# Performance work log

Hardware: AMD Instinct MI355X
Metric: run time of the kernel (lower is better)

The kernel has to match this reference:

```python
import jax, jax.numpy as jnp
import numpy as np

SCORE_THRESHOLD = 0.35
TARGET_CLASS_ID = 0.0
R = 4_194_304  # number of candidate detections (rois)


def setup_inputs() -> dict:
    key = jax.random.key(0)
    k1, k2, k3 = jax.random.split(key, 3)
    class_ids = jax.random.randint(k1, (R,), 0, 4).astype(jnp.float32)
    boxes = jax.random.uniform(k2, (R, 4), dtype=jnp.float32)
    scores = jax.random.uniform(k3, (R,), dtype=jnp.float32)
    detections = jnp.concatenate([class_ids[:, None], boxes, scores[:, None]], axis=1)[None]  # [1, R, 6]
    return {"detections": detections}


def _compact(data, mask):
    # Stable stream compaction with fixed output shape: valid rows moved to the
    # front (original order preserved), invalid tail zero-padded.
    # data: [R, D] float, mask: [R] bool  ->  ([R, D], n_valid)
    order = jnp.argsort(jnp.logical_not(mask), stable=True)  # valid (False-key) first
    sel = jnp.take(data, order, axis=0)
    n = jnp.sum(mask.astype(jnp.int32))
    keep = (jnp.arange(data.shape[0]) < n)[:, None]
    return jnp.where(keep, sel, jnp.zeros((), data.dtype)), n


def reference(detections):
    # detections: [1, R, 6] = [class_id, x1, y1, x2, y2, score]
    d = detections[0]
    class_ids = d[:, 0]
    scores = d[:, 5]
    valid = (class_ids == TARGET_CLASS_ID) & (scores >= SCORE_THRESHOLD)
    valid_full = scores >= SCORE_THRESHOLD

    sel, n = _compact(d, valid)
    # rois: zero class stub + xyxy (score dropped), [1, R, 5]; padded rows are all-zero
    rois = jnp.concatenate([jnp.zeros((d.shape[0], 1), d.dtype), sel[:, 1:5]], axis=1)[None]

    rois_full, n_full = _compact(d, valid_full)
    rois_full = rois_full[None]  # [1, R, 6]

    return rois, rois_full, n, n_full
```

## Files before the change

kernel.cpp:

```cpp
#include <hip/hip_runtime.h>

typedef unsigned int uint32;
typedef unsigned long long uint64;

#define BLOCK 256
#define IPT 16
#define CHUNK (BLOCK * IPT)
#define SCORE_THR 0.35f

__device__ inline void block_reduce2(uint32& a, uint32& b) {
    int tid = threadIdx.x;
    int wave = tid >> 6, lane = tid & 63;
    for (int off = 32; off > 0; off >>= 1) {
        a += __shfl_down(a, off, 64);
        b += __shfl_down(b, off, 64);
    }
    __shared__ uint32 ra[BLOCK / 64], rb[BLOCK / 64];
    if (lane == 0) { ra[wave] = a; rb[wave] = b; }
    __syncthreads();
    uint32 sa = 0, sb = 0;
    for (int w = 0; w < BLOCK / 64; ++w) { sa += ra[w]; sb += rb[w]; }
    a = sa; b = sb;
}

__global__ void count_kernel(const float* __restrict__ det,
                             uint32* __restrict__ c0, uint32* __restrict__ c1,
                             int R) {
    int tid = threadIdx.x;
    long long base = (long long)blockIdx.x * CHUNK;
    uint32 cnt0 = 0, cnt1 = 0;

    if (base + CHUNK <= R) {
        const float4* d4 = (const float4*)det + base * 6 / 4;
        for (int it = 0; it < IPT / 2; ++it) {
            const float4* p = d4 + (long long)it * (BLOCK * 3) + 3 * tid;
            float4 f0 = p[0], f1 = p[1], f2 = p[2];
            bool mA1 = (f1.y >= SCORE_THR);
            bool mA0 = mA1 && (f0.x == 0.0f);
            bool mB1 = (f2.w >= SCORE_THR);
            bool mB0 = mB1 && (f1.z == 0.0f);
            cnt1 += (mA1 ? 1u : 0u) + (mB1 ? 1u : 0u);
            cnt0 += (mA0 ? 1u : 0u) + (mB0 ? 1u : 0u);
        }
    } else {
        for (int i = 0; i < IPT; ++i) {
            long long row = base + (long long)i * BLOCK + tid;
            if (row < R) {
                float c = det[row * 6 + 0];
                float s = det[row * 6 + 5];
                bool m1 = (s >= SCORE_THR);
                bool m0 = m1 && (c == 0.0f);
                cnt1 += m1 ? 1u : 0u;
                cnt0 += m0 ? 1u : 0u;
            }
        }
    }

    block_reduce2(cnt0, cnt1);
    if (tid == 0) { c0[blockIdx.x] = cnt0; c1[blockIdx.x] = cnt1; }
}

__global__ void scatter_zero_kernel(const float* __restrict__ det,
                                    float* __restrict__ rois, float* __restrict__ roisf,
                                    const uint32* __restrict__ c0, const uint32* __restrict__ c1,
                                    float* __restrict__ out_n,
                                    int R, int NB) {
    int tid = threadIdx.x;
    int wave = tid >> 6, lane = tid & 63;
    int bid = blockIdx.x;

    uint32 pre0 = 0, pre1 = 0, tot0 = 0, tot1 = 0;
    for (int j = tid; j < NB; j += BLOCK) {
        uint32 a = c0[j], b = c1[j];
        tot0 += a; tot1 += b;
        if (j < bid) { pre0 += a; pre1 += b; }
    }
    for (int off = 32; off > 0; off >>= 1) {
        pre0 += __shfl_down(pre0, off, 64);
        pre1 += __shfl_down(pre1, off, 64);
        tot0 += __shfl_down(tot0, off, 64);
        tot1 += __shfl_down(tot1, off, 64);
    }
    __shared__ uint32 lp0[4], lp1[4], lt0[4], lt1[4];
    if (lane == 0) { lp0[wave] = pre0; lp1[wave] = pre1; lt0[wave] = tot0; lt1[wave] = tot1; }
    __syncthreads();
    pre0 = lp0[0] + lp0[1] + lp0[2] + lp0[3];
    pre1 = lp1[0] + lp1[1] + lp1[2] + lp1[3];
    tot0 = lt0[0] + lt0[1] + lt0[2] + lt0[3];
    tot1 = lt1[0] + lt1[1] + lt1[2] + lt1[3];

    if (bid == 0 && tid == 0) {
        out_n[0] = (float)tot0;
        out_n[1] = (float)tot1;
    }

    __shared__ uint32 wc0[2][4], wc1[2][4];
    uint32 run0 = pre0, run1 = pre1;
    long long base = (long long)bid * CHUNK;
    uint64 ltmask = (1ull << lane) - 1ull;

    if (base + CHUNK <= R) {
        const float4* d4 = (const float4*)det + base * 6 / 4;
        for (int it = 0; it < IPT / 2; ++it) {
            const float4* p = d4 + (long long)it * (BLOCK * 3) + 3 * tid;
            float4 f0 = p[0], f1 = p[1], f2 = p[2];
            bool mA1 = (f1.y >= SCORE_THR);
            bool mA0 = mA1 && (f0.x == 0.0f);
            bool mB1 = (f2.w >= SCORE_THR);
            bool mB0 = mB1 && (f1.z == 0.0f);

            uint64 bA0 = __ballot(mA0), bA1 = __ballot(mA1);
            uint64 bB0 = __ballot(mB0), bB1 = __ballot(mB1);

            int buf = it & 1;
            if (lane == 0) {
                wc0[buf][wave] = (uint32)(__popcll(bA0) + __popcll(bB0));
                wc1[buf][wave] = (uint32)(__popcll(bA1) + __popcll(bB1));
            }
            __syncthreads();
            uint32 wp0 = 0, wp1 = 0, bt0 = 0, bt1 = 0;
            for (int w = 0; w < 4; ++w) {
                uint32 a = wc0[buf][w], b = wc1[buf][w];
                bt0 += a; bt1 += b;
                if (w < wave) { wp0 += a; wp1 += b; }
            }
            uint32 rA0 = run0 + wp0 + (uint32)(__popcll(bA0 & ltmask) + __popcll(bB0 & ltmask));
            uint32 rB0 = rA0 + (mA0 ? 1u : 0u);
            uint32 rA1 = run1 + wp1 + (uint32)(__popcll(bA1 & ltmask) + __popcll(bB1 & ltmask));
            uint32 rB1 = rA1 + (mA1 ? 1u : 0u);

            if (mA0) {
                float* q = rois + (long long)rA0 * 5;
                q[0] = 0.0f; q[1] = f0.y; q[2] = f0.z; q[3] = f0.w; q[4] = f1.x;
            }
            if (mB0) {
                float* q = rois + (long long)rB0 * 5;
                q[0] = 0.0f; q[1] = f1.w; q[2] = f2.x; q[3] = f2.y; q[4] = f2.z;
            }
            if (mA1) {
                float* q = roisf + (long long)rA1 * 6;
                q[0] = f0.x; q[1] = f0.y; q[2] = f0.z; q[3] = f0.w; q[4] = f1.x; q[5] = f1.y;
            }
            if (mB1) {
                float* q = roisf + (long long)rB1 * 6;
                q[0] = f1.z; q[1] = f1.w; q[2] = f2.x; q[3] = f2.y; q[4] = f2.z; q[5] = f2.w;
            }
            run0 += bt0; run1 += bt1;
        }
    } else {
        for (int i = 0; i < IPT; ++i) {
            long long row = base + (long long)i * BLOCK + tid;
            bool m0 = false, m1 = false;
            float d0 = 0, d1 = 0, d2 = 0, d3 = 0, d4v = 0, d5 = 0;
            if (row < R) {
                const float* pp = det + row * 6;
                d0 = pp[0]; d1 = pp[1]; d2 = pp[2]; d3 = pp[3]; d4v = pp[4]; d5 = pp[5];
                m1 = (d5 >= SCORE_THR);
                m0 = m1 && (d0 == 0.0f);
            }
            uint64 b0 = __ballot(m0), b1 = __ballot(m1);
            int buf = i & 1;
            if (lane == 0) {
                wc0[buf][wave] = (uint32)__popcll(b0);
                wc1[buf][wave] = (uint32)__popcll(b1);
            }
            __syncthreads();
            uint32 wp0 = 0, wp1 = 0, bt0 = 0, bt1 = 0;
            for (int w = 0; w < 4; ++w) {
                uint32 a = wc0[buf][w], b = wc1[buf][w];
                bt0 += a; bt1 += b;
                if (w < wave) { wp0 += a; wp1 += b; }
            }
            if (m0) {
                uint32 pos = run0 + wp0 + (uint32)__popcll(b0 & ltmask);
                float* q = rois + (long long)pos * 5;
                q[0] = 0.0f; q[1] = d1; q[2] = d2; q[3] = d3; q[4] = d4v;
            }
            if (m1) {
                uint32 pos = run1 + wp1 + (uint32)__popcll(b1 & ltmask);
                float* q = roisf + (long long)pos * 6;
                q[0] = d0; q[1] = d1; q[2] = d2; q[3] = d3; q[4] = d4v; q[5] = d5;
            }
            run0 += bt0; run1 += bt1;
        }
    }

    long long z0 = (long long)R * 5 - (long long)tot0 * 5;
    long long z1 = (long long)R * 6 - (long long)tot1 * 6;
    long long total = z0 + z1;
    float* zb0 = rois + (long long)tot0 * 5;
    float* zb1 = roisf + (long long)tot1 * 6;
    long long idx = (long long)bid * BLOCK + tid;
    long long stride = (long long)NB * BLOCK;
    for (long long k = idx; k < total; k += stride) {
        if (k < z0) zb0[k] = 0.0f;
        else        zb1[k - z0] = 0.0f;
    }
}

extern "C" void kernel_launch(void* const* d_in, const int* in_sizes, int n_in,
                              void* d_out, int out_size, void* d_ws, size_t ws_size,
                              hipStream_t stream) {
    const float* det = (const float*)d_in[0];
    float* out = (float*)d_out;
    int R = in_sizes[0] / 6;
    int NB = (R + CHUNK - 1) / CHUNK;

    uint32* ws = (uint32*)d_ws;
    uint32* c0 = ws;
    uint32* c1 = ws + NB;

    float* rois  = out;
    float* roisf = out + (long long)R * 5;
    float* nout  = out + (long long)R * 11;

    count_kernel<<<NB, BLOCK, 0, stream>>>(det, c0, c1, R);
    scatter_zero_kernel<<<NB, BLOCK, 0, stream>>>(det, rois, roisf, c0, c1, nout, R, NB);
}
```

Measured before the change: 294.3 us.

## Stage compacted rows in shared memory for coalesced writes; vectorize zero fill

In the scatter kernel, each iteration's selected rows are first written into double-buffered LDS staging arrays at block-local offsets. The block then copies them out to global memory with contiguous, coalesced stores, replacing the scattered per-thread 5/6-float row writes. The tail zero fill now uses aligned float4 stores in place of scalar stores. In exchange it adds an extra __syncthreads per iteration and about 45KB of shared memory per block, which may lower occupancy.

```diff
diff --git a/kernel.cpp b/kernel.cpp
--- a/kernel.cpp
+++ b/kernel.cpp
@@ -6,27 +6,14 @@
 #define BLOCK 256
 #define IPT 16
 #define CHUNK (BLOCK * IPT)
+#define RPI 512
 #define SCORE_THR 0.35f
-
-__device__ inline void block_reduce2(uint32& a, uint32& b) {
-    int tid = threadIdx.x;
-    int wave = tid >> 6, lane = tid & 63;
-    for (int off = 32; off > 0; off >>= 1) {
-        a += __shfl_down(a, off, 64);
-        b += __shfl_down(b, off, 64);
-    }
-    __shared__ uint32 ra[BLOCK / 64], rb[BLOCK / 64];
-    if (lane == 0) { ra[wave] = a; rb[wave] = b; }
-    __syncthreads();
-    uint32 sa = 0, sb = 0;
-    for (int w = 0; w < BLOCK / 64; ++w) { sa += ra[w]; sb += rb[w]; }
-    a = sa; b = sb;
-}
 
 __global__ void count_kernel(const float* __restrict__ det,
                              uint32* __restrict__ c0, uint32* __restrict__ c1,
                              int R) {
     int tid = threadIdx.x;
+    int wave = tid >> 6, lane = tid & 63;
     long long base = (long long)blockIdx.x * CHUNK;
     uint32 cnt0 = 0, cnt1 = 0;
 
@@ -56,8 +43,32 @@
         }
     }
 
-    block_reduce2(cnt0, cnt1);
-    if (tid == 0) { c0[blockIdx.x] = cnt0; c1[blockIdx.x] = cnt1; }
+    for (int off = 32; off > 0; off >>= 1) {
+        cnt0 += __shfl_down(cnt0, off, 64);
+        cnt1 += __shfl_down(cnt1, off, 64);
+    }
+    __shared__ uint32 ra[4], rb[4];
+    if (lane == 0) { ra[wave] = cnt0; rb[wave] = cnt1; }
+    __syncthreads();
+    if (tid == 0) {
+        c0[blockIdx.x] = ra[0] + ra[1] + ra[2] + ra[3];
+        c1[blockIdx.x] = rb[0] + rb[1] + rb[2] + rb[3];
+    }
+}
+
+__device__ inline void zero_region(float* p, long long n,
+                                   long long gtid, long long gstride) {
+    if (n <= 0) return;
+    long long head = ((4 - (((size_t)p >> 2) & 3)) & 3);
+    if (head > n) head = n;
+    if (gtid < head) p[gtid] = 0.0f;
+    long long n4 = (n - head) >> 2;
+    float4* b = (float4*)(p + head);
+    float4 z4 = make_float4(0.f, 0.f, 0.f, 0.f);
+    for (long long k = gtid; k < n4; k += gstride) b[k] = z4;
+    long long done = head + (n4 << 2);
+    long long rem = n - done;
+    if (gtid < rem) p[done + gtid] = 0.0f;
 }
 
 __global__ void scatter_zero_kernel(const float* __restrict__ det,
@@ -95,6 +106,8 @@
     }
 
     __shared__ uint32 wc0[2][4], wc1[2][4];
+    __shared__ float st0[2][RPI * 5];
+    __shared__ float st1[2][RPI * 6];
     uint32 run0 = pre0, run1 = pre1;
     long long base = (long long)bid * CHUNK;
     uint64 ltmask = (1ull << lane) - 1ull;
@@ -102,6 +115,7 @@
     if (base + CHUNK <= R) {
         const float4* d4 = (const float4*)det + base * 6 / 4;
         for (int it = 0; it < IPT / 2; ++it) {
+            int buf = it & 1;
             const float4* p = d4 + (long long)it * (BLOCK * 3) + 3 * tid;
             float4 f0 = p[0], f1 = p[1], f2 = p[2];
             bool mA1 = (f1.y >= SCORE_THR);
@@ -112,7 +126,6 @@
             uint64 bA0 = __ballot(mA0), bA1 = __ballot(mA1);
             uint64 bB0 = __ballot(mB0), bB1 = __ballot(mB1);
 
-            int buf = it & 1;
             if (lane == 0) {
                 wc0[buf][wave] = (uint32)(__popcll(bA0) + __popcll(bB0));
                 wc1[buf][wave] = (uint32)(__popcll(bA1) + __popcll(bB1));
@@ -124,27 +137,34 @@
                 bt0 += a; bt1 += b;
                 if (w < wave) { wp0 += a; wp1 += b; }
             }
-            uint32 rA0 = run0 + wp0 + (uint32)(__popcll(bA0 & ltmask) + __popcll(bB0 & ltmask));
-            uint32 rB0 = rA0 + (mA0 ? 1u : 0u);
-            uint32 rA1 = run1 + wp1 + (uint32)(__popcll(bA1 & ltmask) + __popcll(bB1 & ltmask));
-            uint32 rB1 = rA1 + (mA1 ? 1u : 0u);
+            uint32 lA0 = wp0 + (uint32)(__popcll(bA0 & ltmask) + __popcll(bB0 & ltmask));
+            uint32 lB0 = lA0 + (mA0 ? 1u : 0u);
+            uint32 lA1 = wp1 + (uint32)(__popcll(bA1 & ltmask) + __popcll(bB1 & ltmask));
+            uint32 lB1 = lA1 + (mA1 ? 1u : 0u);
 
             if (mA0) {
-                float* q = rois + (long long)rA0 * 5;
-                q[0] = 0.0f; q[1] = f0.y; q[2] = f0.z; q[3] = f0.w; q[4] = f1.x;
+                float* s = &st0[buf][lA0 * 5];
+                s[0] = 0.0f; s[1] = f0.y; s[2] = f0.z; s[3] = f0.w; s[4] = f1.x;
             }
             if (mB0) {
-                float* q = rois + (long long)rB0 * 5;
-                q[0] = 0.0f; q[1] = f1.w; q[2] = f2.x; q[3] = f2.y; q[4] = f2.z;
+                float* s = &st0[buf][lB0 * 5];
+                s[0] = 0.0f; s[1] = f1.w; s[2] = f2.x; s[3] = f2.y; s[4] = f2.z;
             }
             if (mA1) {
-                float* q = roisf + (long long)rA1 * 6;
-                q[0] = f0.x; q[1] = f0.y; q[2] = f0.z; q[3] = f0.w; q[4] = f1.x; q[5] = f1.y;
+                float* s = &st1[buf][lA1 * 6];
+                s[0] = f0.x; s[1] = f0.y; s[2] = f0.z; s[3] = f0.w; s[4] = f1.x; s[5] = f1.y;
             }
             if (mB1) {
-                float* q = roisf + (long long)rB1 * 6;
-                q[0] = f1.z; q[1] = f1.w; q[2] = f2.x; q[3] = f2.y; q[4] = f2.z; q[5] = f2.w;
-            }
+                float* s = &st1[buf][lB1 * 6];
+                s[0] = f1.z; s[1] = f1.w; s[2] = f2.x; s[3] = f2.y; s[4] = f2.z; s[5] = f2.w;
+            }
+            __syncthreads();
+
+            uint32 N0 = bt0 * 5, N1 = bt1 * 6;
+            float* g0 = rois + (long long)run0 * 5;
+            float* g1 = roisf + (long long)run1 * 6;
+            for (uint32 j = tid; j < N0; j += BLOCK) g0[j] = st0[buf][j];
+            for (uint32 j = tid; j < N1; j += BLOCK) g1[j] = st1[buf][j];
             run0 += bt0; run1 += bt1;
         }
     } else {
@@ -182,20 +202,16 @@
                 q[0] = d0; q[1] = d1; q[2] = d2; q[3] = d3; q[4] = d4v; q[5] = d5;
             }
             run0 += bt0; run1 += bt1;
-        }
-    }
-
-    long long z0 = (long long)R * 5 - (long long)tot0 * 5;
-    long long z1 = (long long)R * 6 - (long long)tot1 * 6;
-    long long total = z0 + z1;
-    float* zb0 = rois + (long long)tot0 * 5;
-    float* zb1 = roisf + (long long)tot1 * 6;
-    long long idx = (long long)bid * BLOCK + tid;
-    long long stride = (long long)NB * BLOCK;
-    for (long long k = idx; k < total; k += stride) {
-        if (k < z0) zb0[k] = 0.0f;
-        else        zb1[k - z0] = 0.0f;
-    }
+            __syncthreads();
+        }
+    }
+
+    long long gtid = (long long)bid * BLOCK + tid;
+    long long gstride = (long long)NB * BLOCK;
+    zero_region(rois + (long long)tot0 * 5, (long long)(R - (long long)tot0) * 5,
+                gtid, gstride);
+    zero_region(roisf + (long long)tot1 * 6, (long long)(R - (long long)tot1) * 6,
+                gtid, gstride);
 }
 
 extern "C" void kernel_launch(void* const* d_in, const int* in_sizes, int n_in,
```

New measurement: 286.9 us. 1.03x faster.
